# Optimization experiments

Hardware: AMD Instinct MI355X
Metric: run time of the kernel (lower is better)

## Reference

```python
import jax, jax.numpy as jnp
import numpy as np

B, T, IN, H, OUT = 64, 512, 256, 512, 256


def setup_inputs() -> dict:
    key = jax.random.key(0)
    ks = jax.random.split(key, 12)
    s_in = 1.0 / np.sqrt(H)  # PyTorch RNN init scale (uniform +-1/sqrt(H))
    u = lambda k, shape: jax.random.uniform(k, shape, jnp.float32, -s_in, s_in)
    return {
        "x": jax.random.normal(ks[0], (B, T, IN), jnp.float32),
        "W_ih0": u(ks[1], (H, IN)),
        "W_hh0": u(ks[2], (H, H)),
        "b_ih0": u(ks[3], (H,)),
        "b_hh0": u(ks[4], (H,)),
        "W_ih1": u(ks[5], (H, H)),
        "W_hh1": u(ks[6], (H, H)),
        "b_ih1": u(ks[7], (H,)),
        "b_hh1": u(ks[8], (H,)),
        "W_out": u(ks[9], (OUT, H)),
        "b_out": u(ks[10], (OUT,)),
    }


def _rnn_layer(seq, W_ih, W_hh, b_ih, b_hh):
    # seq: [B, T, D_in] -> outputs [B, T, H], last hidden [B, H]
    # Precompute input projection for all steps (one big GEMM).
    xp = jnp.einsum('btd,hd->bth', seq, W_ih) + b_ih + b_hh  # [B, T, H]
    xp_t = jnp.swapaxes(xp, 0, 1)  # [T, B, H] for scan over time
    h0 = jnp.zeros((seq.shape[0], W_hh.shape[0]), seq.dtype)

    def step(h, xpt):
        h = jnp.tanh(xpt + h @ W_hh.T)
        return h, h

    h_last, hs = jax.lax.scan(step, h0, xp_t)
    return jnp.swapaxes(hs, 0, 1), h_last


def reference(x, W_ih0, W_hh0, b_ih0, b_hh0, W_ih1, W_hh1, b_ih1, b_hh1, W_out, b_out):
    out0, _ = _rnn_layer(x, W_ih0, W_hh0, b_ih0, b_hh0)
    _, h_last = _rnn_layer(out0, W_ih1, W_hh1, b_ih1, b_hh1)
    return h_last @ W_out.T + b_out  # [B, OUT]
```

## Files before the change

### kernel.cpp

```cpp
#include <hip/hip_runtime.h>
#include <cmath>

#define B_   64
#define T_   512
#define IN_  256
#define H_   512
#define OUT_ 256
#define M_   (B_*T_)

typedef __bf16 bf16x4 __attribute__((ext_vector_type(4)));
typedef __bf16 bf16x8 __attribute__((ext_vector_type(8)));
typedef float  f32x4  __attribute__((ext_vector_type(4)));
typedef unsigned long long u64;

static __device__ __forceinline__ void split_f32(float x, __bf16 &hi, __bf16 &lo) {
    unsigned u  = __float_as_uint(x);
    unsigned hu = u & 0xffff0000u;
    hi = __builtin_bit_cast(__bf16, (unsigned short)(hu >> 16));
    lo = (__bf16)(x - __uint_as_float(hu));
}

__global__ void split_arr(const float* __restrict__ src, __bf16* __restrict__ hi,
                          __bf16* __restrict__ lo, int n) {
    int i = blockIdx.x * 256 + threadIdx.x;
    if (i < n) { __bf16 h, l; split_f32(src[i], h, l); hi[i] = h; lo[i] = l; }
}

__global__ void bias_comb(const float* __restrict__ a, const float* __restrict__ b,
                          float* __restrict__ o, int n) {
    int i = blockIdx.x * 256 + threadIdx.x;
    if (i < n) o[i] = a[i] + b[i];
}

#define GBM 128
#define GBN 64
#define GBK 32
#define LDA 40

__global__ __launch_bounds__(256) void gemm_xp(
    const float* __restrict__ A, const __bf16* __restrict__ Whi,
    const __bf16* __restrict__ Wlo, const float* __restrict__ bias,
    float* __restrict__ C, int K)
{
    __shared__ __bf16 sAhi[GBM*LDA], sAlo[GBM*LDA], sBhi[GBN*LDA], sBlo[GBN*LDA];
    const int tid = threadIdx.x;
    const int m0 = blockIdx.y * GBM, n0 = blockIdx.x * GBN;
    const int wave = tid >> 6, lane = tid & 63, lm = lane & 15, q = lane >> 4;

    f32x4 acc[2][4];
#pragma unroll
    for (int i = 0; i < 2; ++i)
#pragma unroll
        for (int j = 0; j < 4; ++j) acc[i][j] = (f32x4){0.f,0.f,0.f,0.f};

    for (int k0 = 0; k0 < K; k0 += GBK) {
        __syncthreads();
#pragma unroll
        for (int i = 0; i < 4; ++i) {
            int c = tid + i * 256;
            int row = c >> 3, pos = c & 7;
            float4 v = *(const float4*)(&A[(size_t)(m0+row)*K + k0 + pos*4]);
            __bf16 h0,l0,h1,l1,h2,l2,h3,l3;
            split_f32(v.x,h0,l0); split_f32(v.y,h1,l1);
            split_f32(v.z,h2,l2); split_f32(v.w,h3,l3);
            *(bf16x4*)(&sAhi[row*LDA + pos*4]) = (bf16x4){h0,h1,h2,h3};
            *(bf16x4*)(&sAlo[row*LDA + pos*4]) = (bf16x4){l0,l1,l2,l3};
        }
        {
            int row = tid >> 2, pos = (tid & 3) * 8;
            *(bf16x8*)(&sBhi[row*LDA + pos]) =
                *(const bf16x8*)(&Whi[(size_t)(n0+row)*K + k0 + pos]);
            *(bf16x8*)(&sBlo[row*LDA + pos]) =
                *(const bf16x8*)(&Wlo[(size_t)(n0+row)*K + k0 + pos]);
        }
        __syncthreads();

        bf16x8 ah[2], al[2], bh[4], bl[4];
#pragma unroll
        for (int mt = 0; mt < 2; ++mt) {
            int r = wave*32 + mt*16 + lm;
            ah[mt] = *(const bf16x8*)(&sAhi[r*LDA + q*8]);
            al[mt] = *(const bf16x8*)(&sAlo[r*LDA + q*8]);
        }
#pragma unroll
        for (int nt = 0; nt < 4; ++nt) {
            int r = nt*16 + lm;
            bh[nt] = *(const bf16x8*)(&sBhi[r*LDA + q*8]);
            bl[nt] = *(const bf16x8*)(&sBlo[r*LDA + q*8]);
        }
#pragma unroll
        for (int mt = 0; mt < 2; ++mt)
#pragma unroll
            for (int nt = 0; nt < 4; ++nt) {
                acc[mt][nt] = __builtin_amdgcn_mfma_f32_16x16x32_bf16(ah[mt], bh[nt], acc[mt][nt], 0,0,0);
                acc[mt][nt] = __builtin_amdgcn_mfma_f32_16x16x32_bf16(ah[mt], bl[nt], acc[mt][nt], 0,0,0);
                acc[mt][nt] = __builtin_amdgcn_mfma_f32_16x16x32_bf16(al[mt], bh[nt], acc[mt][nt], 0,0,0);
            }
    }
#pragma unroll
    for (int mt = 0; mt < 2; ++mt)
#pragma unroll
        for (int nt = 0; nt < 4; ++nt)
#pragma unroll
            for (int r = 0; r < 4; ++r) {
                int m = m0 + wave*32 + mt*16 + q*4 + r;
                int n = n0 + nt*16 + lm;
                C[(size_t)m*H_ + n] = acc[mt][nt][r] + bias[n];
            }
}

#define RLDA 520
#define RDEP 8

#define MMA16(ACC, WH, WL) do { \
    _Pragma("unroll") \
    for (int kt = 0; kt < 16; ++kt) { \
        bf16x8 ah = *(const bf16x8*)(&sAhi[lm*RLDA + kt*32 + q*8]); \
        bf16x8 al = *(const bf16x8*)(&sAlo[lm*RLDA + kt*32 + q*8]); \
        ACC = __builtin_amdgcn_mfma_f32_16x16x32_bf16(ah, WH[kt], ACC, 0,0,0); \
        ACC = __builtin_amdgcn_mfma_f32_16x16x32_bf16(ah, WL[kt], ACC, 0,0,0); \
        ACC = __builtin_amdgcn_mfma_f32_16x16x32_bf16(al, WH[kt], ACC, 0,0,0); \
    } } while (0)

__global__ __launch_bounds__(256, 1) void rnn_fused(
    const float* __restrict__ xp0,
    const __bf16* __restrict__ w0hi, const __bf16* __restrict__ w0lo,
    const __bf16* __restrict__ wphi, const __bf16* __restrict__ wplo,
    const __bf16* __restrict__ w1hi, const __bf16* __restrict__ w1lo,
    const float* __restrict__ bias1,
    unsigned* __restrict__ h0ring,
    u64*      __restrict__ xp1ring,
    unsigned* __restrict__ h1ring,
    float* __restrict__ hlast,
    int* __restrict__ flags)
{
    __shared__ __bf16 sAhi[16*RLDA], sAlo[16*RLDA];
    const int tid  = threadIdx.x;
    const int role = blockIdx.x >> 5;
    const int sub  = blockIdx.x & 31;
    const int g    = sub >> 3;
    const int c    = sub & 7;
    const int m0g  = g * 16;
    const int n0   = c * 64;
    const int wave = tid >> 6, lane = tid & 63, lm = lane & 15, q = lane >> 4;
    const int ncol = n0 + wave*16 + lm;
    const int srow = tid >> 4, sseg = tid & 15;

    int* const flag0 = flags + g*16;
    int* const flag1 = flags + 64 + g*16;

    const __bf16* Wh = role ? w1hi : w0hi;
    const __bf16* Wl = role ? w1lo : w0lo;
    bf16x8 wh[16], wl[16], ph[16], pl[16];
#pragma unroll
    for (int kt = 0; kt < 16; ++kt) {
        wh[kt] = *(const bf16x8*)(&Wh[(size_t)ncol*H_ + kt*32 + q*8]);
        wl[kt] = *(const bf16x8*)(&Wl[(size_t)ncol*H_ + kt*32 + q*8]);
        asm volatile("" : "+v"(wh[kt]), "+v"(wl[kt]));
    }
    if (role == 0) {
#pragma unroll
        for (int kt = 0; kt < 16; ++kt) {
            ph[kt] = *(const bf16x8*)(&wphi[(size_t)ncol*H_ + kt*32 + q*8]);
            pl[kt] = *(const bf16x8*)(&wplo[(size_t)ncol*H_ + kt*32 + q*8]);
            asm volatile("" : "+v"(ph[kt]), "+v"(pl[kt]));
        }
    }

    auto stage = [&](const unsigned* base) {
        const u64* row = (const u64*)(base + (size_t)(m0g + srow)*H_);
        __bf16* dh = &sAhi[srow*RLDA];
        __bf16* dl = &sAlo[srow*RLDA];
        u64 vv[16];
#pragma unroll
        for (int j = 0; j < 16; ++j)
            vv[j] = __hip_atomic_load(&row[sseg + j*16], __ATOMIC_RELAXED,
                                      __HIP_MEMORY_SCOPE_AGENT);
#pragma unroll
        for (int j = 0; j < 16; ++j) {
            unsigned pa = (unsigned)vv[j], pb = (unsigned)(vv[j] >> 32);
            int c0 = (sseg + j*16) * 2;
            *(unsigned*)(dh + c0) = (pa >> 16) | (pb & 0xffff0000u);
            *(unsigned*)(dl + c0) = (pa & 0xffffu) | (pb << 16);
        }
    };
    auto pollge = [&](int* f, int tv) {
        for (;;) {
            int v = __hip_atomic_load(&f[lane & 7], __ATOMIC_RELAXED,
                                      __HIP_MEMORY_SCOPE_AGENT);
            if (__all(v >= tv)) break;
            __builtin_amdgcn_s_sleep(1);
        }
    };

    if (role == 0) {
        const float b1 = bias1[ncol];
        for (int t = 0; t <= T_; ++t) {
            float xr[4];
            if (t < T_) {
#pragma unroll
                for (int r = 0; r < 4; ++r)
                    xr[r] = xp0[((size_t)(m0g + q*4 + r)*T_ + t)*H_ + ncol];
            }
            if (t) pollge(flag0, t);
            __syncthreads();
            stage(h0ring + (size_t)(t & 7)*(B_*H_));
            __syncthreads();

            if (t < T_) {
                f32x4 acc = (f32x4){0.f,0.f,0.f,0.f};
                MMA16(acc, wh, wl);
                unsigned* dst = h0ring + (size_t)((t+1) & 7)*(B_*H_);
#pragma unroll
                for (int r = 0; r < 4; ++r) {
                    float hv = tanhf(xr[r] + acc[r]);
                    __bf16 hh, hl; split_f32(hv, hh, hl);
                    unsigned pk = ((unsigned)__builtin_bit_cast(unsigned short, hh) << 16)
                                |  (unsigned)__builtin_bit_cast(unsigned short, hl);
                    __hip_atomic_store(&dst[(size_t)(m0g + q*4 + r)*H_ + ncol], pk,
                                       __ATOMIC_RELAXED, __HIP_MEMORY_SCOPE_AGENT);
                }
                __syncthreads();
                if (tid == 0)
                    __hip_atomic_store(&flag0[c], t+1, __ATOMIC_RELEASE,
                                       __HIP_MEMORY_SCOPE_AGENT);
            }
            if (t >= 1) {
                f32x4 a2 = (f32x4){0.f,0.f,0.f,0.f};
                MMA16(a2, ph, pl);
                if (t >= RDEP + 1)
                    pollge(flag1, t - RDEP);
                u64* dst = xp1ring + (size_t)((t-1) & 7)*(B_*H_);
#pragma unroll
                for (int r = 0; r < 4; ++r) {
                    u64 pv = ((u64)(unsigned)t << 32) | __float_as_uint(a2[r] + b1);
                    __hip_atomic_store(&dst[(size_t)(m0g + q*4 + r)*H_ + ncol], pv,
                                       __ATOMIC_RELAXED, __HIP_MEMORY_SCOPE_AGENT);
                }
            }
        }
    } else {
        for (int t = 0; t < T_; ++t) {
            const u64* xs = xp1ring + (size_t)(t & 7)*(B_*H_);
            u64 xv[4];
#pragma unroll
            for (int r = 0; r < 4; ++r)
                xv[r] = __hip_atomic_load(&xs[(size_t)(m0g + q*4 + r)*H_ + ncol],
                                          __ATOMIC_RELAXED, __HIP_MEMORY_SCOPE_AGENT);
            if (t) pollge(flag1, t);
            __syncthreads();
            stage(h1ring + (size_t)(t & 1)*(B_*H_));
            __syncthreads();

            f32x4 acc = (f32x4){0.f,0.f,0.f,0.f};
            MMA16(acc, wh, wl);

#pragma unroll
            for (int r = 0; r < 4; ++r) {
                while ((unsigned)(xv[r] >> 32) != (unsigned)(t+1)) {
                    __builtin_amdgcn_s_sleep(1);
                    xv[r] = __hip_atomic_load(&xs[(size_t)(m0g + q*4 + r)*H_ + ncol],
                                              __ATOMIC_RELAXED, __HIP_MEMORY_SCOPE_AGENT);
                }
            }
            unsigned* dst = h1ring + (size_t)((t+1) & 1)*(B_*H_);
#pragma unroll
            for (int r = 0; r < 4; ++r) {
                int m = m0g + q*4 + r;
                float hv = tanhf(__uint_as_float((unsigned)xv[r]) + acc[r]);
                __bf16 hh, hl; split_f32(hv, hh, hl);
                unsigned pk = ((unsigned)__builtin_bit_cast(unsigned short, hh) << 16)
                            |  (unsigned)__builtin_bit_cast(unsigned short, hl);
                __hip_atomic_store(&dst[(size_t)m*H_ + ncol], pk,
                                   __ATOMIC_RELAXED, __HIP_MEMORY_SCOPE_AGENT);
                if (t == T_-1) hlast[(size_t)m*H_ + ncol] = hv;
            }
            __syncthreads();
            if (tid == 0)
                __hip_atomic_store(&flag1[c], t+1, __ATOMIC_RELEASE,
                                   __HIP_MEMORY_SCOPE_AGENT);
        }
    }
}

__global__ __launch_bounds__(256) void out_proj(
    const float* __restrict__ hlast, const float* __restrict__ Wout,
    const float* __restrict__ bout, float* __restrict__ out)
{
    __shared__ float sh[H_];
    int b = blockIdx.x;
    for (int i = threadIdx.x; i < H_; i += 256) sh[i] = hlast[(size_t)b*H_ + i];
    __syncthreads();
    int o = threadIdx.x;
    const float* wr = &Wout[(size_t)o*H_];
    float acc = 0.f;
#pragma unroll 4
    for (int k = 0; k < H_; k += 4) {
        float4 wv = *(const float4*)(&wr[k]);
        acc += wv.x*sh[k] + wv.y*sh[k+1] + wv.z*sh[k+2] + wv.w*sh[k+3];
    }
    out[(size_t)b*OUT_ + o] = bout[o] + acc;
}

extern "C" void kernel_launch(void* const* d_in, const int* in_sizes, int n_in,
                              void* d_out, int out_size, void* d_ws, size_t ws_size,
                              hipStream_t stream)
{
    const float* x    = (const float*)d_in[0];
    const float* Wih0 = (const float*)d_in[1];
    const float* Whh0 = (const float*)d_in[2];
    const float* bih0 = (const float*)d_in[3];
    const float* bhh0 = (const float*)d_in[4];
    const float* Wih1 = (const float*)d_in[5];
    const float* Whh1 = (const float*)d_in[6];
    const float* bih1 = (const float*)d_in[7];
    const float* bhh1 = (const float*)d_in[8];
    const float* Wout = (const float*)d_in[9];
    const float* bout = (const float*)d_in[10];

    char* w = (char*)d_ws;
    size_t off = 0;
    auto alloc = [&](size_t bytes) -> void* {
        void* p = w + off; off = (off + bytes + 255) & ~(size_t)255; return p;
    };
    float*  xp     = (float*) alloc((size_t)M_*H_*4);
    __bf16* wih0hi = (__bf16*)alloc((size_t)H_*IN_*2);
    __bf16* wih0lo = (__bf16*)alloc((size_t)H_*IN_*2);
    __bf16* whh0hi = (__bf16*)alloc((size_t)H_*H_*2);
    __bf16* whh0lo = (__bf16*)alloc((size_t)H_*H_*2);
    __bf16* wih1hi = (__bf16*)alloc((size_t)H_*H_*2);
    __bf16* wih1lo = (__bf16*)alloc((size_t)H_*H_*2);
    __bf16* whh1hi = (__bf16*)alloc((size_t)H_*H_*2);
    __bf16* whh1lo = (__bf16*)alloc((size_t)H_*H_*2);
    float*  bias0  = (float*) alloc(H_*4);
    float*  bias1  = (float*) alloc(H_*4);
    size_t zstart = off;
    unsigned* h0ring = (unsigned*)alloc((size_t)RDEP*B_*H_*4);
    u64*      xp1ring= (u64*)     alloc((size_t)RDEP*B_*H_*8);
    unsigned* h1ring = (unsigned*)alloc((size_t)2*B_*H_*4);
    int*      flags  = (int*)     alloc(512);
    size_t zlen = off - zstart;
    float*  hlast  = (float*) alloc((size_t)B_*H_*4);

    hipMemsetAsync(w + zstart, 0, zlen, stream);

    split_arr<<<(H_*IN_+255)/256, 256, 0, stream>>>(Wih0, wih0hi, wih0lo, H_*IN_);
    split_arr<<<(H_*H_ +255)/256, 256, 0, stream>>>(Whh0, whh0hi, whh0lo, H_*H_);
    split_arr<<<(H_*H_ +255)/256, 256, 0, stream>>>(Wih1, wih1hi, wih1lo, H_*H_);
    split_arr<<<(H_*H_ +255)/256, 256, 0, stream>>>(Whh1, whh1hi, whh1lo, H_*H_);
    bias_comb<<<2, 256, 0, stream>>>(bih0, bhh0, bias0, H_);
    bias_comb<<<2, 256, 0, stream>>>(bih1, bhh1, bias1, H_);

    dim3 ggrid(H_/GBN, M_/GBM);
    gemm_xp<<<ggrid, 256, 0, stream>>>(x, wih0hi, wih0lo, bias0, xp, IN_);

    rnn_fused<<<64, 256, 0, stream>>>(xp, whh0hi, whh0lo, wih1hi, wih1lo,
                                      whh1hi, whh1lo, bias1,
                                      h0ring, xp1ring, h1ring, hlast, flags);

    out_proj<<<B_, 256, 0, stream>>>(hlast, Wout, bout, (float*)d_out);
}
```

Before: 2.776 ms.

## Use per-wave completion flags and stream layer-1 input weights from memory

Each wave now publishes its own progress flag after waiting on its stores, instead of a block-wide barrier followed by a single release store. Consumers poll all 32 wave flags of a group, which removes one __syncthreads from each step of the serial recurrence. The layer-1 input-projection weights are no longer held in registers but loaded from global memory on every step, freeing VGPRs at the cost of repeated L2 traffic. The release ordering now rests on s_waitcnt plus relaxed stores, which risks memory-ordering subtleties.

```diff
diff --git a/kernel.cpp b/kernel.cpp
--- a/kernel.cpp
+++ b/kernel.cpp
@@ -111,6 +111,7 @@
 
 #define RLDA 520
 #define RDEP 8
+#define BH   (B_*H_)
 
 #define MMA16(ACC, WH, WL) do { \
     _Pragma("unroll") \
@@ -120,6 +121,18 @@
         ACC = __builtin_amdgcn_mfma_f32_16x16x32_bf16(ah, WH[kt], ACC, 0,0,0); \
         ACC = __builtin_amdgcn_mfma_f32_16x16x32_bf16(ah, WL[kt], ACC, 0,0,0); \
         ACC = __builtin_amdgcn_mfma_f32_16x16x32_bf16(al, WH[kt], ACC, 0,0,0); \
+    } } while (0)
+
+#define MMA16G(ACC, PH, PL) do { \
+    _Pragma("unroll") \
+    for (int kt = 0; kt < 16; ++kt) { \
+        bf16x8 bh = *(const bf16x8*)(&PH[(size_t)ncol*H_ + kt*32 + q*8]); \
+        bf16x8 bl = *(const bf16x8*)(&PL[(size_t)ncol*H_ + kt*32 + q*8]); \
+        bf16x8 ah = *(const bf16x8*)(&sAhi[lm*RLDA + kt*32 + q*8]); \
+        bf16x8 al = *(const bf16x8*)(&sAlo[lm*RLDA + kt*32 + q*8]); \
+        ACC = __builtin_amdgcn_mfma_f32_16x16x32_bf16(ah, bh, ACC, 0,0,0); \
+        ACC = __builtin_amdgcn_mfma_f32_16x16x32_bf16(ah, bl, ACC, 0,0,0); \
+        ACC = __builtin_amdgcn_mfma_f32_16x16x32_bf16(al, bh, ACC, 0,0,0); \
     } } while (0)
 
 __global__ __launch_bounds__(256, 1) void rnn_fused(
@@ -146,26 +159,19 @@
     const int ncol = n0 + wave*16 + lm;
     const int srow = tid >> 4, sseg = tid & 15;
 
-    int* const flag0 = flags + g*16;
-    int* const flag1 = flags + 64 + g*16;
+    int* const gf     = flags + (role*4 + g)*32;
+    int* const myflag = gf + c*4 + wave;
+    int* const bp1c   = flags + (1*4 + g)*32 + c*4;
 
     const __bf16* Wh = role ? w1hi : w0hi;
     const __bf16* Wl = role ? w1lo : w0lo;
-    bf16x8 wh[16], wl[16], ph[16], pl[16];
+    bf16x8 wh[16], wl[16];
 #pragma unroll
     for (int kt = 0; kt < 16; ++kt) {
         wh[kt] = *(const bf16x8*)(&Wh[(size_t)ncol*H_ + kt*32 + q*8]);
         wl[kt] = *(const bf16x8*)(&Wl[(size_t)ncol*H_ + kt*32 + q*8]);
         asm volatile("" : "+v"(wh[kt]), "+v"(wl[kt]));
     }
-    if (role == 0) {
-#pragma unroll
-        for (int kt = 0; kt < 16; ++kt) {
-            ph[kt] = *(const bf16x8*)(&wphi[(size_t)ncol*H_ + kt*32 + q*8]);
-            pl[kt] = *(const bf16x8*)(&wplo[(size_t)ncol*H_ + kt*32 + q*8]);
-            asm volatile("" : "+v"(ph[kt]), "+v"(pl[kt]));
-        }
-    }
 
     auto stage = [&](const unsigned* base) {
         const u64* row = (const u64*)(base + (size_t)(m0g + srow)*H_);
@@ -184,13 +190,18 @@
             *(unsigned*)(dl + c0) = (pa & 0xffffu) | (pb << 16);
         }
     };
-    auto pollge = [&](int* f, int tv) {
+    auto pollall = [&](int tv) {
         for (;;) {
-            int v = __hip_atomic_load(&f[lane & 7], __ATOMIC_RELAXED,
+            int v = __hip_atomic_load(&gf[lane & 31], __ATOMIC_RELAXED,
                                       __HIP_MEMORY_SCOPE_AGENT);
             if (__all(v >= tv)) break;
             __builtin_amdgcn_s_sleep(1);
         }
+    };
+    auto signal = [&](int tv) {
+        asm volatile("s_waitcnt vmcnt(0)" ::: "memory");
+        if (lane == 0)
+            __hip_atomic_store(myflag, tv, __ATOMIC_RELAXED, __HIP_MEMORY_SCOPE_AGENT);
     };
 
     if (role == 0) {
@@ -202,15 +213,15 @@
                 for (int r = 0; r < 4; ++r)
                     xr[r] = xp0[((size_t)(m0g + q*4 + r)*T_ + t)*H_ + ncol];
             }
-            if (t) pollge(flag0, t);
+            if (t) pollall(t);
             __syncthreads();
-            stage(h0ring + (size_t)(t & 7)*(B_*H_));
+            stage(h0ring + (size_t)(t & 7)*BH);
             __syncthreads();
 
             if (t < T_) {
                 f32x4 acc = (f32x4){0.f,0.f,0.f,0.f};
                 MMA16(acc, wh, wl);
-                unsigned* dst = h0ring + (size_t)((t+1) & 7)*(B_*H_);
+                unsigned* dst = h0ring + (size_t)((t+1) & 7)*BH;
 #pragma unroll
                 for (int r = 0; r < 4; ++r) {
                     float hv = tanhf(xr[r] + acc[r]);
@@ -220,17 +231,20 @@
                     __hip_atomic_store(&dst[(size_t)(m0g + q*4 + r)*H_ + ncol], pk,
                                        __ATOMIC_RELAXED, __HIP_MEMORY_SCOPE_AGENT);
                 }
-                __syncthreads();
-                if (tid == 0)
-                    __hip_atomic_store(&flag0[c], t+1, __ATOMIC_RELEASE,
-                                       __HIP_MEMORY_SCOPE_AGENT);
+                signal(t+1);
             }
             if (t >= 1) {
                 f32x4 a2 = (f32x4){0.f,0.f,0.f,0.f};
-                MMA16(a2, ph, pl);
-                if (t >= RDEP + 1)
-                    pollge(flag1, t - RDEP);
-                u64* dst = xp1ring + (size_t)((t-1) & 7)*(B_*H_);
+                MMA16G(a2, wphi, wplo);
+                if (t >= RDEP + 1) {
+                    for (;;) {
+                        int v = __hip_atomic_load(&bp1c[lane & 3], __ATOMIC_RELAXED,
+                                                  __HIP_MEMORY_SCOPE_AGENT);
+                        if (__all(v >= t - RDEP)) break;
+                        __builtin_amdgcn_s_sleep(1);
+                    }
+                }
+                u64* dst = xp1ring + (size_t)((t-1) & 7)*BH;
 #pragma unroll
                 for (int r = 0; r < 4; ++r) {
                     u64 pv = ((u64)(unsigned)t << 32) | __float_as_uint(a2[r] + b1);
@@ -241,15 +255,15 @@
         }
     } else {
         for (int t = 0; t < T_; ++t) {
-            const u64* xs = xp1ring + (size_t)(t & 7)*(B_*H_);
+            const u64* xs = xp1ring + (size_t)(t & 7)*BH;
             u64 xv[4];
 #pragma unroll
             for (int r = 0; r < 4; ++r)
                 xv[r] = __hip_atomic_load(&xs[(size_t)(m0g + q*4 + r)*H_ + ncol],
                                           __ATOMIC_RELAXED, __HIP_MEMORY_SCOPE_AGENT);
-            if (t) pollge(flag1, t);
+            if (t) pollall(t);
             __syncthreads();
-            stage(h1ring + (size_t)(t & 1)*(B_*H_));
+            stage(h1ring + (size_t)(t & 1)*BH);
             __syncthreads();
 
             f32x4 acc = (f32x4){0.f,0.f,0.f,0.f};
@@ -263,7 +277,7 @@
                                               __ATOMIC_RELAXED, __HIP_MEMORY_SCOPE_AGENT);
                 }
             }
-            unsigned* dst = h1ring + (size_t)((t+1) & 1)*(B_*H_);
+            unsigned* dst = h1ring + (size_t)((t+1) & 1)*BH;
 #pragma unroll
             for (int r = 0; r < 4; ++r) {
                 int m = m0g + q*4 + r;
@@ -275,10 +289,7 @@
                                    __ATOMIC_RELAXED, __HIP_MEMORY_SCOPE_AGENT);
                 if (t == T_-1) hlast[(size_t)m*H_ + ncol] = hv;
             }
-            __syncthreads();
-            if (tid == 0)
-                __hip_atomic_store(&flag1[c], t+1, __ATOMIC_RELEASE,
-                                   __HIP_MEMORY_SCOPE_AGENT);
+            signal(t+1);
         }
     }
 }
@@ -338,7 +349,7 @@
     unsigned* h0ring = (unsigned*)alloc((size_t)RDEP*B_*H_*4);
     u64*      xp1ring= (u64*)     alloc((size_t)RDEP*B_*H_*8);
     unsigned* h1ring = (unsigned*)alloc((size_t)2*B_*H_*4);
-    int*      flags  = (int*)     alloc(512);
+    int*      flags  = (int*)     alloc(1024);
     size_t zlen = off - zstart;
     float*  hlast  = (float*) alloc((size_t)B_*H_*4);
 
```

Measured after the change: 3.656 ms. 31.7% more time.
